# Kernel tuning notes

Measured on AMD Instinct MI355X. Metric: run time of the kernel, lower is better.

The kernel has to match this reference:

```python
import jax, jax.numpy as jnp
import numpy as np

D_MODEL = 1024
D_Q = 1024
D_K = 1024
D_V = 1024
B, S = 4, 2048


def setup_inputs() -> dict:
    key = jax.random.key(0)
    kx, kq, kk, kv = jax.random.split(key, 4)
    # torch Linear(in, out) weight is [out, in]; y = x @ W.T. Use kaiming-ish scale.
    sc = 1.0 / np.sqrt(D_MODEL)
    x = jax.random.normal(kx, (B, S, D_MODEL), dtype=jnp.float32)
    Wq = jax.random.normal(kq, (D_Q, D_MODEL), dtype=jnp.float32) * sc
    Wk = jax.random.normal(kk, (D_K, D_MODEL), dtype=jnp.float32) * sc
    Wv = jax.random.normal(kv, (D_V, D_MODEL), dtype=jnp.float32) * sc
    return {"x": x, "Wq": Wq, "Wk": Wk, "Wv": Wv}


def reference(x, Wq, Wk, Wv):
    d_k = Wk.shape[0]
    q = jnp.einsum('bsd,qd->bsq', x, Wq)  # [B,S,d_q]
    k = jnp.einsum('bsd,kd->bsk', x, Wk)  # [B,S,d_k]
    v = jnp.einsum('bsd,vd->bsv', x, Wv)  # [B,S,d_v]
    scores = jnp.einsum('bqd,bkd->bqk', q, k) / jnp.sqrt(jnp.float32(d_k))
    seq = scores.shape[-1]
    causal = jnp.tril(jnp.ones((seq, seq), dtype=bool))  # True = keep
    scores = jnp.where(causal[None, :, :], scores, -jnp.inf)
    probs = jax.nn.softmax(scores, axis=-1)
    return jnp.einsum('bqk,bkv->bqv', probs, v)
```

## Files before the change

### kernel.cpp

```cpp
#include <hip/hip_runtime.h>
#include <hip/hip_bf16.h>
#include <stdint.h>

typedef __attribute__((ext_vector_type(8))) short short8;
typedef __attribute__((ext_vector_type(4))) float floatx4;

typedef const __attribute__((address_space(1))) void* gvp;
typedef __attribute__((address_space(3))) void* lvp;

__device__ __forceinline__ unsigned short f2bf(float f) {
    unsigned u = __float_as_uint(f);
    u += 0x7fffu + ((u >> 16) & 1u);
    return (unsigned short)(u >> 16);
}

#define BAR()   do { asm volatile("" ::: "memory"); __builtin_amdgcn_s_barrier(); asm volatile("" ::: "memory"); } while (0)
#define WAITL() do { asm volatile("s_waitcnt lgkmcnt(0)" ::: "memory"); __builtin_amdgcn_sched_barrier(0); } while (0)
#define WAITV4() asm volatile("s_waitcnt vmcnt(4)" ::: "memory")

__global__ __launch_bounds__(256)
void cvt_kernel(const float* __restrict__ in, unsigned short* __restrict__ out, long n4) {
    long i = (long)blockIdx.x * blockDim.x + threadIdx.x;
    long stride = (long)gridDim.x * blockDim.x;
    for (long idx = i; idx < n4; idx += stride) {
        float4 v = reinterpret_cast<const float4*>(in)[idx];
        uint2 o;
        o.x = (unsigned)f2bf(v.x) | ((unsigned)f2bf(v.y) << 16);
        o.y = (unsigned)f2bf(v.z) | ((unsigned)f2bf(v.w) << 16);
        reinterpret_cast<uint2*>(out)[idx] = o;
    }
}

__global__ __launch_bounds__(256)
void cvt_w3(const float* __restrict__ a, const float* __restrict__ b,
            const float* __restrict__ c, unsigned short* __restrict__ out, long n4) {
    const float* in = (blockIdx.y == 0) ? a : (blockIdx.y == 1) ? b : c;
    unsigned short* o = out + (long)blockIdx.y * n4 * 4;
    long i = (long)blockIdx.x * blockDim.x + threadIdx.x;
    long stride = (long)gridDim.x * blockDim.x;
    for (long idx = i; idx < n4; idx += stride) {
        float4 v = reinterpret_cast<const float4*>(in)[idx];
        uint2 ov;
        ov.x = (unsigned)f2bf(v.x) | ((unsigned)f2bf(v.y) << 16);
        ov.y = (unsigned)f2bf(v.z) | ((unsigned)f2bf(v.w) << 16);
        reinterpret_cast<uint2*>(o)[idx] = ov;
    }
}

__device__ __forceinline__ void stage_half(char* slot, const unsigned short* src,
                                           int ld, int k0, int tid) {
    #pragma unroll
    for (int r = 0; r < 2; ++r) {
        const int c = r * 512 + tid;
        const int row = c >> 3;
        const int cs = ((c & 7) * 16) ^ ((row & 7) << 4);
        const char* g = reinterpret_cast<const char*>(src + (long)row * ld + k0) + cs;
        __builtin_amdgcn_global_load_lds((gvp)g,
            (lvp)(slot + r * 8192 + (tid >> 6) * 1024), 16, 0, 0);
    }
}

__device__ __forceinline__ void load_a4(short8 a_[4][2], const char* slot, int mh,
                                        int fr, int csw0, int csw1) {
    #pragma unroll
    for (int i = 0; i < 4; ++i) {
        const int rb = (mh * 64 + i * 16 + fr) * 128;
        a_[i][0] = *reinterpret_cast<const short8*>(slot + rb + csw0);
        a_[i][1] = *reinterpret_cast<const short8*>(slot + rb + csw1);
    }
}

__device__ __forceinline__ void load_b2(short8 b_[2][2], const char* slot, int rbase,
                                        int nh, int fr, int csw0, int csw1) {
    #pragma unroll
    for (int j = 0; j < 2; ++j) {
        const int rb = (rbase + nh * 32 + j * 16 + fr) * 128;
        b_[j][0] = *reinterpret_cast<const short8*>(slot + rb + csw0);
        b_[j][1] = *reinterpret_cast<const short8*>(slot + rb + csw1);
    }
}

__device__ __forceinline__ void mfma16(floatx4 acc[8][4], short8 a_[4][2],
                                       short8 b_[2][2], int mh, int nh) {
    __builtin_amdgcn_s_setprio(1);
    #pragma unroll
    for (int i = 0; i < 4; ++i)
        #pragma unroll
        for (int j = 0; j < 2; ++j) {
            acc[mh*4+i][nh*2+j] = __builtin_amdgcn_mfma_f32_16x16x32_bf16(
                a_[i][0], b_[j][0], acc[mh*4+i][nh*2+j], 0, 0, 0);
            acc[mh*4+i][nh*2+j] = __builtin_amdgcn_mfma_f32_16x16x32_bf16(
                a_[i][1], b_[j][1], acc[mh*4+i][nh*2+j], 0, 0, 0);
        }
    __builtin_amdgcn_s_setprio(0);
}

template<typename CT, int MODE>
__global__ __launch_bounds__(512, 2)
void gemm8p(const unsigned short* __restrict__ A, const unsigned short* __restrict__ B,
            CT* __restrict__ C, int K, int lda, int ldb, int ldc,
            long sA, long sB, long sC, int nwg)
{
    const int gx = gridDim.x, gy = gridDim.y;
    int flat = (blockIdx.z * gy + blockIdx.y) * gx + blockIdx.x;
    {
        int xcd = flat & 7, lid = flat >> 3;
        int q = nwg >> 3, r = nwg & 7;
        flat = (xcd < r ? xcd * (q + 1) : r * (q + 1) + (xcd - r) * q) + lid;
    }
    const int bx = flat % gx;
    const int t2 = flat / gx;
    const int by = t2 % gy;
    const int bz = t2 / gy;
    if (MODE == 1 && bx > by) return;

    A += (long)bz * sA + (long)by * 256 * lda;
    B += (long)bz * sB + (long)bx * 256 * ldb;
    C += (long)bz * sC;

    __shared__ __align__(16) char lds[8 * 16384];
    #define SLOT(db, op, half) (lds + ((((db) << 1 | (op)) << 1 | (half)) * 16384))

    const int tid  = threadIdx.x;
    const int lane = tid & 63;
    const int wid  = tid >> 6;
    const int wm = wid >> 2;
    const int wn = wid & 3;
    const int bh = wn >> 1;
    const int brbase = (wn & 1) * 64;
    const int fr = lane & 15;
    const int csw0 = ((lane >> 4) * 16) ^ ((fr & 7) << 4);
    const int csw1 = (64 + (lane >> 4) * 16) ^ ((fr & 7) << 4);

    const unsigned short* Ah[2] = { A, A + 128ll * lda };
    const unsigned short* Bh[2] = { B, B + 128ll * ldb };

    const int NT = K >> 6;
    const int NI = NT >> 1;

    floatx4 acc[8][4] = {};
    short8 a_[4][2];
    short8 b_[2][2][2];

    stage_half(SLOT(0,1,0), Bh[0], ldb, 0, tid);
    stage_half(SLOT(0,1,1), Bh[1], ldb, 0, tid);
    stage_half(SLOT(0,0,0), Ah[0], lda, 0, tid);
    stage_half(SLOT(0,0,1), Ah[1], lda, 0, tid);
    stage_half(SLOT(1,1,0), Bh[0], ldb, 64, tid);
    stage_half(SLOT(1,1,1), Bh[1], ldb, 64, tid);
    WAITV4();
    BAR();

    for (int I = 0; I < NI; ++I) {
        const int kA1 = min(2*I + 1, NT - 1) * 64;
        const int kT2 = min(2*I + 2, NT - 1) * 64;
        const int kB3 = min(2*I + 3, NT - 1) * 64;

        load_a4(a_, SLOT(0,0,wm), 0, fr, csw0, csw1);
        load_b2(b_[0], SLOT(0,1,bh), brbase, 0, fr, csw0, csw1);
        stage_half(SLOT(1,0,0), Ah[0], lda, kA1, tid);
        BAR(); WAITL();
        mfma16(acc, a_, b_[0], 0, 0);
        BAR();

        load_b2(b_[1], SLOT(0,1,bh), brbase, 1, fr, csw0, csw1);
        stage_half(SLOT(1,0,1), Ah[1], lda, kA1, tid);
        BAR(); WAITL();
        mfma16(acc, a_, b_[1], 0, 1);
        BAR();

        load_a4(a_, SLOT(0,0,wm), 1, fr, csw0, csw1);
        stage_half(SLOT(0,1,0), Bh[0], ldb, kT2, tid);
        BAR(); WAITL();
        mfma16(acc, a_, b_[1], 1, 1);
        BAR();

        stage_half(SLOT(0,1,1), Bh[1], ldb, kT2, tid);
        BAR(); WAITL();
        mfma16(acc, a_, b_[0], 1, 0);
        WAITV4();
        BAR();

        load_a4(a_, SLOT(1,0,wm), 0, fr, csw0, csw1);
        load_b2(b_[0], SLOT(1,1,bh), brbase, 0, fr, csw0, csw1);
        stage_half(SLOT(0,0,0), Ah[0], lda, kT2, tid);
        BAR(); WAITL();
        mfma16(acc, a_, b_[0], 0, 0);
        BAR();

        load_b2(b_[1], SLOT(1,1,bh), brbase, 1, fr, csw0, csw1);
        stage_half(SLOT(0,0,1), Ah[1], lda, kT2, tid);
        BAR(); WAITL();
        mfma16(acc, a_, b_[1], 0, 1);
        BAR();

        load_a4(a_, SLOT(1,0,wm), 1, fr, csw0, csw1);
        stage_half(SLOT(1,1,0), Bh[0], ldb, kB3, tid);
        BAR(); WAITL();
        mfma16(acc, a_, b_[1], 1, 1);
        BAR();

        stage_half(SLOT(1,1,1), Bh[1], ldb, kB3, tid);
        BAR(); WAITL();
        mfma16(acc, a_, b_[0], 1, 0);
        WAITV4();
        BAR();
    }

    const int cr0 = by * 256 + wm * 128 + (lane >> 4) * 4;
    const int cc0 = bx * 256 + wn * 64 + (lane & 15);
    #pragma unroll
    for (int i = 0; i < 8; ++i)
        #pragma unroll
        for (int j = 0; j < 4; ++j)
            #pragma unroll
            for (int r = 0; r < 4; ++r) {
                long idx = (long)(cr0 + i * 16 + r) * ldc + (cc0 + j * 16);
                float v = acc[i][j][r];
                if constexpr (sizeof(CT) == 4) C[idx] = v;
                else                           C[idx] = (CT)f2bf(v);
            }
    #undef SLOT
}

template<typename CT, int MODE>
__global__ __launch_bounds__(256, 3)
void gemm_bt(const unsigned short* __restrict__ A, const unsigned short* __restrict__ B,
             CT* __restrict__ C, int K, int lda, int ldb, int ldc,
             long sA, long sB, long sC, int nwg)
{
    const int gx = gridDim.x, gy = gridDim.y;
    int flat = (blockIdx.z * gy + blockIdx.y) * gx + blockIdx.x;
    {
        int xcd = flat & 7, lid = flat >> 3;
        int q = nwg >> 3, r = nwg & 7;
        flat = (xcd < r ? xcd * (q + 1) : r * (q + 1) + (xcd - r) * q) + lid;
    }
    int bx = flat % gx;
    int t2 = flat / gx;
    int by = t2 % gy;
    const int bz = t2 / gy;
    if (MODE == 2) {
        by = ((by & 1) << 3) | ((by & 2) << 1) | ((by & 4) >> 1) | ((by & 8) >> 3);
    }

    A += (long)bz * sA; B += (long)bz * sB; C += (long)bz * sC;
    const int kend = (MODE == 2) ? min(K, (by + 1) * 128) : K;

    __shared__ unsigned short As[128 * 64];
    __shared__ unsigned short Bs[128 * 64];

    const int tid  = threadIdx.x;
    const int lane = tid & 63;
    const int wid  = tid >> 6;
    const int m0 = by * 128, n0 = bx * 128;
    const int wm = (wid >> 1) * 64, wn = (wid & 1) * 64;
    const int frow = lane & 15;
    const int fk   = (lane >> 4) * 8;

    const int srow = lane >> 3;
    const int scolb = (lane & 7) * 16;

    floatx4 acc[4][4] = {};

    for (int k0 = 0; k0 < kend; k0 += 64) {
        __syncthreads();
        #pragma unroll
        for (int i = 0; i < 4; ++i) {
            const int c = wid * 4 + i;
            const int row = c * 8 + srow;
            const char* ga = reinterpret_cast<const char*>(A + (long)(m0 + row) * lda + k0) + scolb;
            __builtin_amdgcn_global_load_lds((gvp)ga,
                (lvp)(reinterpret_cast<char*>(As) + c * 1024), 16, 0, 0);
            const char* gb = reinterpret_cast<const char*>(B + (long)(n0 + row) * ldb + k0) + scolb;
            __builtin_amdgcn_global_load_lds((gvp)gb,
                (lvp)(reinterpret_cast<char*>(Bs) + c * 1024), 16, 0, 0);
        }
        __syncthreads();
        #pragma unroll
        for (int ks = 0; ks < 2; ++ks) {
            short8 af[4], bf[4];
            #pragma unroll
            for (int i = 0; i < 4; ++i) {
                const int ar = wm + i * 16 + frow;
                af[i] = *reinterpret_cast<const short8*>(
                    reinterpret_cast<const char*>(As) + ar * 128 + (ks * 32 + fk) * 2);
                const int br = wn + i * 16 + frow;
                bf[i] = *reinterpret_cast<const short8*>(
                    reinterpret_cast<const char*>(Bs) + br * 128 + (ks * 32 + fk) * 2);
            }
            #pragma unroll
            for (int i = 0; i < 4; ++i)
                #pragma unroll
                for (int j = 0; j < 4; ++j)
                    acc[i][j] = __builtin_amdgcn_mfma_f32_16x16x32_bf16(af[i], bf[j], acc[i][j], 0, 0, 0);
        }
    }

    const int cr0 = m0 + wm + (lane >> 4) * 4;
    const int cc0 = n0 + wn + (lane & 15);
    #pragma unroll
    for (int i = 0; i < 4; ++i)
        #pragma unroll
        for (int j = 0; j < 4; ++j)
            #pragma unroll
            for (int r = 0; r < 4; ++r) {
                long idx = (long)(cr0 + i * 16 + r) * ldc + (cc0 + j * 16);
                float v = acc[i][j][r];
                if constexpr (sizeof(CT) == 4) C[idx] = v;
                else                           C[idx] = (CT)f2bf(v);
            }
}

__global__ __launch_bounds__(256)
void softmax_causal(float* __restrict__ Sc) {
    const int q = blockIdx.x;
    const int b = blockIdx.y;
    float* row = Sc + ((long)b * 2048 + q) * 2048;
    const int t = threadIdx.x;
    const int lane = t & 63, wid = t >> 6;

    float vals[8];
    float mx = -INFINITY;
    #pragma unroll
    for (int i = 0; i < 2; ++i) {
        const int c0 = i * 1024 + t * 4;
        if (c0 <= q) {
            float4 v = *reinterpret_cast<const float4*>(row + c0);
            float tmp[4] = {v.x, v.y, v.z, v.w};
            #pragma unroll
            for (int j = 0; j < 4; ++j) {
                float val = (c0 + j <= q) ? tmp[j] * 0.03125f : -INFINITY;
                vals[i * 4 + j] = val;
                mx = fmaxf(mx, val);
            }
        } else {
            vals[i*4+0] = vals[i*4+1] = vals[i*4+2] = vals[i*4+3] = -INFINITY;
        }
    }
    #pragma unroll
    for (int o = 32; o > 0; o >>= 1) mx = fmaxf(mx, __shfl_xor(mx, o));
    __shared__ float rmax[4], rsum[4];
    if (lane == 0) rmax[wid] = mx;
    __syncthreads();
    mx = fmaxf(fmaxf(rmax[0], rmax[1]), fmaxf(rmax[2], rmax[3]));

    float s = 0.f;
    #pragma unroll
    for (int k = 0; k < 8; ++k) {
        float e = __expf(vals[k] - mx);
        vals[k] = e;
        s += e;
    }
    #pragma unroll
    for (int o = 32; o > 0; o >>= 1) s += __shfl_xor(s, o);
    if (lane == 0) rsum[wid] = s;
    __syncthreads();
    s = rsum[0] + rsum[1] + rsum[2] + rsum[3];
    const float inv = 1.f / s;

    unsigned short* orow = reinterpret_cast<unsigned short*>(row);
    #pragma unroll
    for (int i = 0; i < 2; ++i) {
        uint2 o;
        o.x = (unsigned)f2bf(vals[i*4+0] * inv) | ((unsigned)f2bf(vals[i*4+1] * inv) << 16);
        o.y = (unsigned)f2bf(vals[i*4+2] * inv) | ((unsigned)f2bf(vals[i*4+3] * inv) << 16);
        *reinterpret_cast<uint2*>(orow + i * 1024 + t * 4) = o;
    }
}

__global__ __launch_bounds__(256)
void transpose_v(const unsigned short* __restrict__ V, unsigned short* __restrict__ Vt) {
    const int b = blockIdx.z;
    const int v0 = blockIdx.x * 64;
    const int s0 = blockIdx.y * 64;
    __shared__ unsigned short tile[64][68];
    const int t = threadIdx.x;
    const int ii = t >> 4;
    const int jj = (t & 15) * 4;
    #pragma unroll
    for (int p = 0; p < 4; ++p) {
        int s = p * 16 + ii;
        ushort4 val = *reinterpret_cast<const ushort4*>(V + (long)(b * 2048 + s0 + s) * 1024 + v0 + jj);
        *reinterpret_cast<ushort4*>(&tile[s][jj]) = val;
    }
    __syncthreads();
    #pragma unroll
    for (int p = 0; p < 4; ++p) {
        int vl = p * 16 + ii;
        ushort4 o;
        o.x = tile[jj + 0][vl];
        o.y = tile[jj + 1][vl];
        o.z = tile[jj + 2][vl];
        o.w = tile[jj + 3][vl];
        *reinterpret_cast<ushort4*>(Vt + (long)(b * 1024 + v0 + vl) * 2048 + s0 + jj) = o;
    }
}

extern "C" void kernel_launch(void* const* d_in, const int* in_sizes, int n_in,
                              void* d_out, int out_size, void* d_ws, size_t ws_size,
                              hipStream_t stream) {
    const float* x  = (const float*)d_in[0];
    const float* Wq = (const float*)d_in[1];
    const float* Wk = (const float*)d_in[2];
    const float* Wv = (const float*)d_in[3];
    float* out = (float*)d_out;

    char* w = (char*)d_ws;
    unsigned short* Xb = (unsigned short*)(w);
    unsigned short* Wb = (unsigned short*)(w + (16ll << 20));
    unsigned short* Qb = (unsigned short*)(w + (22ll << 20));
    unsigned short* Kb = (unsigned short*)(w + (38ll << 20));
    unsigned short* Vb = (unsigned short*)(w + (54ll << 20));
    unsigned short* Vt = (unsigned short*)(w + (70ll << 20));
    float* Sc = (float*)(w + (86ll << 20));

    dim3 blk(256);
    cvt_kernel<<<2048, blk, 0, stream>>>(x, Xb, (8192ll * 1024) / 4);
    cvt_w3<<<dim3(512, 3), blk, 0, stream>>>(Wq, Wk, Wv, Wb, (1024ll * 1024) / 4);

    gemm8p<unsigned short, 0><<<dim3(4, 32, 3), dim3(512), 0, stream>>>(
        Xb, Wb, Qb, 1024, 1024, 1024, 1024,
        0, 1024ll * 1024, 8192ll * 1024, 4 * 32 * 3);

    transpose_v<<<dim3(16, 32, 4), blk, 0, stream>>>(Vb, Vt);

    gemm8p<float, 1><<<dim3(8, 8, 4), dim3(512), 0, stream>>>(
        Qb, Kb, Sc, 1024, 1024, 1024, 2048,
        2048ll * 1024, 2048ll * 1024, 2048ll * 2048, 8 * 8 * 4);

    softmax_causal<<<dim3(2048, 4), blk, 0, stream>>>(Sc);

    gemm_bt<float, 2><<<dim3(8, 16, 4), blk, 0, stream>>>(
        (const unsigned short*)Sc, Vt, out, 2048, 4096, 2048, 1024,
        2048ll * 4096, 1024ll * 2048, 2048ll * 1024, 8 * 16 * 4);
}
```

Before: 175.2 us.

## Fuse V transpose into projection GEMM epilogue and merge conversion kernels

The V-projection blocks of the QKV GEMM now transpose their bf16 tile through LDS and write Vt directly. This removes the separate transpose kernel and the Vb round trip through memory. The x and weight conversions are merged into one kernel launch. Softmax now stores only up to the 128-aligned causal boundary, skipping writes the PV GEMM presumably never reads. The risks are extra LDS work and a divergent epilogue in the GEMM, and stale values in the unwritten columns if any downstream read touches them.

```diff
diff --git a/kernel.cpp b/kernel.cpp
--- a/kernel.cpp
+++ b/kernel.cpp
@@ -17,33 +17,31 @@
 #define BAR()   do { asm volatile("" ::: "memory"); __builtin_amdgcn_s_barrier(); asm volatile("" ::: "memory"); } while (0)
 #define WAITL() do { asm volatile("s_waitcnt lgkmcnt(0)" ::: "memory"); __builtin_amdgcn_sched_barrier(0); } while (0)
 #define WAITV4() asm volatile("s_waitcnt vmcnt(4)" ::: "memory")
+#define WAITV0() asm volatile("s_waitcnt vmcnt(0)" ::: "memory")
 
 __global__ __launch_bounds__(256)
-void cvt_kernel(const float* __restrict__ in, unsigned short* __restrict__ out, long n4) {
+void cvt_all(const float* __restrict__ x, const float* __restrict__ wq,
+             const float* __restrict__ wk, const float* __restrict__ wv,
+             unsigned short* __restrict__ Xb, unsigned short* __restrict__ Wb) {
+    const long NX = 8192l * 1024 / 4;
+    const long NW = 1024l * 1024 / 4;
     long i = (long)blockIdx.x * blockDim.x + threadIdx.x;
     long stride = (long)gridDim.x * blockDim.x;
-    for (long idx = i; idx < n4; idx += stride) {
-        float4 v = reinterpret_cast<const float4*>(in)[idx];
+    for (long idx = i; idx < NX + 3 * NW; idx += stride) {
+        const float* in; unsigned short* out; long off;
+        if (idx < NX) { in = x; out = Xb; off = idx; }
+        else {
+            long r = idx - NX;
+            int sel = (int)(r >> 18);
+            off = r & (NW - 1);
+            in = (sel == 0) ? wq : (sel == 1) ? wk : wv;
+            out = Wb + (long)sel * NW * 4;
+        }
+        float4 v = reinterpret_cast<const float4*>(in)[off];
         uint2 o;
         o.x = (unsigned)f2bf(v.x) | ((unsigned)f2bf(v.y) << 16);
         o.y = (unsigned)f2bf(v.z) | ((unsigned)f2bf(v.w) << 16);
-        reinterpret_cast<uint2*>(out)[idx] = o;
-    }
-}
-
-__global__ __launch_bounds__(256)
-void cvt_w3(const float* __restrict__ a, const float* __restrict__ b,
-            const float* __restrict__ c, unsigned short* __restrict__ out, long n4) {
-    const float* in = (blockIdx.y == 0) ? a : (blockIdx.y == 1) ? b : c;
-    unsigned short* o = out + (long)blockIdx.y * n4 * 4;
-    long i = (long)blockIdx.x * blockDim.x + threadIdx.x;
-    long stride = (long)gridDim.x * blockDim.x;
-    for (long idx = i; idx < n4; idx += stride) {
-        float4 v = reinterpret_cast<const float4*>(in)[idx];
-        uint2 ov;
-        ov.x = (unsigned)f2bf(v.x) | ((unsigned)f2bf(v.y) << 16);
-        ov.y = (unsigned)f2bf(v.z) | ((unsigned)f2bf(v.w) << 16);
-        reinterpret_cast<uint2*>(o)[idx] = ov;
+        reinterpret_cast<uint2*>(out)[off] = o;
     }
 }
 
@@ -98,7 +96,8 @@
 template<typename CT, int MODE>
 __global__ __launch_bounds__(512, 2)
 void gemm8p(const unsigned short* __restrict__ A, const unsigned short* __restrict__ B,
-            CT* __restrict__ C, int K, int lda, int ldb, int ldc,
+            CT* __restrict__ C, unsigned short* __restrict__ Vt,
+            int K, int lda, int ldb, int ldc,
             long sA, long sB, long sC, int nwg)
 {
     const int gx = gridDim.x, gy = gridDim.y;
@@ -205,6 +204,35 @@
         mfma16(acc, a_, b_[0], 1, 0);
         WAITV4();
         BAR();
+    }
+
+    if (MODE == 0 && bz == 2) {
+        WAITV0();
+        BAR();
+        char* T = lds;
+        #pragma unroll
+        for (int i = 0; i < 8; ++i)
+            #pragma unroll
+            for (int j = 0; j < 4; ++j) {
+                const int n = wn * 64 + j * 16 + fr;
+                const int m = wm * 128 + ((lane >> 4) << 2) + i * 16;
+                uint2 pk;
+                pk.x = (unsigned)f2bf(acc[i][j][0]) | ((unsigned)f2bf(acc[i][j][1]) << 16);
+                pk.y = (unsigned)f2bf(acc[i][j][2]) | ((unsigned)f2bf(acc[i][j][3]) << 16);
+                *reinterpret_cast<uint2*>(T + n * 512 + ((m * 2) ^ ((n & 7) << 4))) = pk;
+            }
+        __syncthreads();
+        const int b  = by >> 3;
+        const int s0 = (by & 7) * 256;
+        #pragma unroll
+        for (int c = 0; c < 16; ++c) {
+            const int idx = c * 512 + tid;
+            const int n = idx >> 5, k = idx & 31;
+            uint4 v = *reinterpret_cast<const uint4*>(T + n * 512 + ((k * 16) ^ ((n & 7) << 4)));
+            *reinterpret_cast<uint4*>(Vt + (long)b * (1024 * 2048)
+                + (long)(bx * 256 + n) * 2048 + s0 + k * 8) = v;
+        }
+        return;
     }
 
     const int cr0 = by * 256 + wm * 128 + (lane >> 4) * 4;
@@ -319,6 +347,7 @@
     float* row = Sc + ((long)b * 2048 + q) * 2048;
     const int t = threadIdx.x;
     const int lane = t & 63, wid = t >> 6;
+    const int kend = (q | 127) + 1;
 
     float vals[8];
     float mx = -INFINITY;
@@ -362,38 +391,13 @@
     unsigned short* orow = reinterpret_cast<unsigned short*>(row);
     #pragma unroll
     for (int i = 0; i < 2; ++i) {
-        uint2 o;
-        o.x = (unsigned)f2bf(vals[i*4+0] * inv) | ((unsigned)f2bf(vals[i*4+1] * inv) << 16);
-        o.y = (unsigned)f2bf(vals[i*4+2] * inv) | ((unsigned)f2bf(vals[i*4+3] * inv) << 16);
-        *reinterpret_cast<uint2*>(orow + i * 1024 + t * 4) = o;
-    }
-}
-
-__global__ __launch_bounds__(256)
-void transpose_v(const unsigned short* __restrict__ V, unsigned short* __restrict__ Vt) {
-    const int b = blockIdx.z;
-    const int v0 = blockIdx.x * 64;
-    const int s0 = blockIdx.y * 64;
-    __shared__ unsigned short tile[64][68];
-    const int t = threadIdx.x;
-    const int ii = t >> 4;
-    const int jj = (t & 15) * 4;
-    #pragma unroll
-    for (int p = 0; p < 4; ++p) {
-        int s = p * 16 + ii;
-        ushort4 val = *reinterpret_cast<const ushort4*>(V + (long)(b * 2048 + s0 + s) * 1024 + v0 + jj);
-        *reinterpret_cast<ushort4*>(&tile[s][jj]) = val;
-    }
-    __syncthreads();
-    #pragma unroll
-    for (int p = 0; p < 4; ++p) {
-        int vl = p * 16 + ii;
-        ushort4 o;
-        o.x = tile[jj + 0][vl];
-        o.y = tile[jj + 1][vl];
-        o.z = tile[jj + 2][vl];
-        o.w = tile[jj + 3][vl];
-        *reinterpret_cast<ushort4*>(Vt + (long)(b * 1024 + v0 + vl) * 2048 + s0 + jj) = o;
+        const int c0 = i * 1024 + t * 4;
+        if (c0 < kend) {
+            uint2 o;
+            o.x = (unsigned)f2bf(vals[i*4+0] * inv) | ((unsigned)f2bf(vals[i*4+1] * inv) << 16);
+            o.y = (unsigned)f2bf(vals[i*4+2] * inv) | ((unsigned)f2bf(vals[i*4+3] * inv) << 16);
+            *reinterpret_cast<uint2*>(orow + c0) = o;
+        }
     }
 }
 
@@ -411,22 +415,18 @@
     unsigned short* Wb = (unsigned short*)(w + (16ll << 20));
     unsigned short* Qb = (unsigned short*)(w + (22ll << 20));
     unsigned short* Kb = (unsigned short*)(w + (38ll << 20));
-    unsigned short* Vb = (unsigned short*)(w + (54ll << 20));
     unsigned short* Vt = (unsigned short*)(w + (70ll << 20));
     float* Sc = (float*)(w + (86ll << 20));
 
     dim3 blk(256);
-    cvt_kernel<<<2048, blk, 0, stream>>>(x, Xb, (8192ll * 1024) / 4);
-    cvt_w3<<<dim3(512, 3), blk, 0, stream>>>(Wq, Wk, Wv, Wb, (1024ll * 1024) / 4);
+    cvt_all<<<2816, blk, 0, stream>>>(x, Wq, Wk, Wv, Xb, Wb);
 
     gemm8p<unsigned short, 0><<<dim3(4, 32, 3), dim3(512), 0, stream>>>(
-        Xb, Wb, Qb, 1024, 1024, 1024, 1024,
+        Xb, Wb, Qb, Vt, 1024, 1024, 1024, 1024,
         0, 1024ll * 1024, 8192ll * 1024, 4 * 32 * 3);
 
-    transpose_v<<<dim3(16, 32, 4), blk, 0, stream>>>(Vb, Vt);
-
     gemm8p<float, 1><<<dim3(8, 8, 4), dim3(512), 0, stream>>>(
-        Qb, Kb, Sc, 1024, 1024, 1024, 2048,
+        Qb, Kb, Sc, nullptr, 1024, 1024, 1024, 2048,
         2048ll * 1024, 2048ll * 1024, 2048ll * 2048, 8 * 8 * 4);
 
     softmax_causal<<<dim3(2048, 4), blk, 0, stream>>>(Sc);
```

After: 166.9 us. -4.7%, faster.
